# Performance work log

Measured on AMD Instinct MI355X. Metric: run time of the kernel, lower is better.

The kernel has to match this reference:

```python
import jax, jax.numpy as jnp
import numpy as np

N, E, DIN, H, EIN, EH, STEPS = 10000, 100000, 64, 64, 16, 128, 3


def setup_inputs() -> dict:
    key = jax.random.key(0)
    ks = jax.random.split(key, 8)
    n_feat = jax.random.normal(ks[0], (N, DIN), jnp.float32)
    e_feat = jax.random.normal(ks[1], (E, EIN), jnp.float32)
    src = jax.random.randint(ks[2], (E,), 0, N, jnp.int32)
    dst = jax.random.randint(ks[3], (E,), 0, N, jnp.int32)
    W0 = jax.random.normal(ks[4], (DIN, H), jnp.float32) / np.sqrt(DIN)
    b0 = jnp.zeros((H,), jnp.float32)
    We1 = jax.random.normal(ks[5], (EIN, EH), jnp.float32) / np.sqrt(EIN)
    be1 = jnp.zeros((EH,), jnp.float32)
    # small scale so per-edge HxH weight matrices keep activations stable
    We2 = jax.random.normal(ks[6], (EH, H * H), jnp.float32) * 0.02
    be2 = jnp.zeros((H * H,), jnp.float32)
    conv_bias = jnp.zeros((H,), jnp.float32)
    gamma = jnp.ones((H,), jnp.float32)
    beta = jnp.zeros((H,), jnp.float32)
    return {"n_feat": n_feat, "e_feat": e_feat, "src": src, "dst": dst,
            "W0": W0, "b0": b0, "We1": We1, "be1": be1, "We2": We2,
            "be2": be2, "conv_bias": conv_bias, "gamma": gamma, "beta": beta}


def reference(n_feat, e_feat, src, dst, W0, b0, We1, be1, We2, be2, conv_bias, gamma, beta):
    n = n_feat.shape[0]
    h = W0.shape[1]
    out = jax.nn.relu(n_feat @ W0 + b0)  # [N,H]
    # edge network (eval mode: dropout = identity); e_feat is fixed so the
    # per-edge weight matrices are identical each step -> compute once.
    w_edge = (jax.nn.relu(e_feat @ We1 + be1) @ We2 + be2).reshape(-1, h, h)  # [E,H,H]
    for _ in range(STEPS):
        msg = jnp.einsum('ei,eio->eo', out[src], w_edge)  # gather + per-edge matmul
        agg = jax.ops.segment_sum(msg, dst, num_segments=n)  # scatter-sum to dst
        out = jax.nn.relu(agg + conv_bias)
    # BatchNorm1d over nodes (training-mode batch statistics)
    mean = jnp.mean(out, axis=0)
    var = jnp.var(out, axis=0)
    return (out - mean) * jax.lax.rsqrt(var + 1e-5) * gamma + beta
```

## Files before the change

### kernel.cpp

```cpp
#include <hip/hip_runtime.h>
#include <stdint.h>

#define DIN   64
#define HDIM  64
#define EIN   16
#define EHID  128
#define HH    4096
#define TC    8256
#define STEPS 3

typedef short bf16x8 __attribute__((ext_vector_type(8)));
typedef float f32x4  __attribute__((ext_vector_type(4)));

__device__ __forceinline__ unsigned short f32_to_bf16(float f) {
    union { float f; uint32_t u; } v; v.f = f;
    uint32_t r = v.u + 0x7fffu + ((v.u >> 16) & 1u);
    return (unsigned short)(r >> 16);
}
__device__ __forceinline__ float bfu_to_f(unsigned short u) {
    union { uint32_t u; float f; } v; v.u = (uint32_t)u << 16; return v.f;
}

__global__ void k_pro(const float* __restrict__ nf, const float* __restrict__ W0,
                      const float* __restrict__ b0, float* __restrict__ outb,
                      unsigned short* __restrict__ outbf,
                      const float* __restrict__ ef, const float* __restrict__ We1,
                      const float* __restrict__ be1, unsigned short* __restrict__ h,
                      const float* __restrict__ We2, const float* __restrict__ be2,
                      unsigned short* __restrict__ BmatT,
                      const int* __restrict__ src, const int* __restrict__ dst,
                      int* __restrict__ cntS, int* __restrict__ cntD,
                      int n_nodes, int n_edges, int nbN, int nbE, int nbB) {
    __shared__ float smem[DIN * HDIM];
    int b = blockIdx.x, tid = threadIdx.x;
    if (b < nbN) {
        for (int i = tid; i < DIN * HDIM; i += 256) smem[i] = W0[i];
        __syncthreads();
        int node = b * 4 + (tid >> 6);
        int o = tid & 63;
        if (node >= n_nodes) return;
        float xr = nf[node * DIN + o];
        float acc = b0[o];
#pragma unroll 8
        for (int i = 0; i < DIN; ++i)
            acc += __shfl(xr, i, 64) * smem[i * HDIM + o];
        float v = fmaxf(acc, 0.f);
        outb[node * HDIM + o] = v;
        outbf[node * HDIM + o] = f32_to_bf16(v);
    } else if (b < nbN + nbE) {
        int wave = tid >> 6, lane = tid & 63;
        int r = lane & 15, q = lane >> 4;
        int e0 = (b - nbN) * 64 + wave * 16;
        if (e0 >= n_edges) return;
        bf16x8 afr = (bf16x8){};
        bf16x8 bfr[8];
#pragma unroll
        for (int nt = 0; nt < 8; ++nt) bfr[nt] = (bf16x8){};
        if (q < 2) {
            int ea = e0 + r; if (ea >= n_edges) ea = n_edges - 1;
            const float* xa = ef + (size_t)ea * EIN + q * 8;
#pragma unroll
            for (int j = 0; j < 8; ++j) afr[j] = (short)f32_to_bf16(xa[j]);
#pragma unroll
            for (int nt = 0; nt < 8; ++nt)
#pragma unroll
                for (int j = 0; j < 8; ++j)
                    bfr[nt][j] = (short)f32_to_bf16(We1[(q * 8 + j) * EHID + nt * 16 + r]);
        }
        f32x4 acc[8];
#pragma unroll
        for (int nt = 0; nt < 8; ++nt)
            acc[nt] = __builtin_amdgcn_mfma_f32_16x16x32_bf16(afr, bfr[nt], (f32x4){}, 0, 0, 0);
        float bias[8];
#pragma unroll
        for (int nt = 0; nt < 8; ++nt) bias[nt] = be1[nt * 16 + r];
#pragma unroll
        for (int rg = 0; rg < 4; ++rg) {
            int e = e0 + q * 4 + rg;
            if (e >= n_edges) continue;
            ushort4 pk0, pk1;
            pk0.x = f32_to_bf16(fmaxf(acc[0][rg] + bias[0], 0.f));
            pk0.y = f32_to_bf16(fmaxf(acc[1][rg] + bias[1], 0.f));
            pk0.z = f32_to_bf16(fmaxf(acc[2][rg] + bias[2], 0.f));
            pk0.w = f32_to_bf16(fmaxf(acc[3][rg] + bias[3], 0.f));
            pk1.x = f32_to_bf16(fmaxf(acc[4][rg] + bias[4], 0.f));
            pk1.y = f32_to_bf16(fmaxf(acc[5][rg] + bias[5], 0.f));
            pk1.z = f32_to_bf16(fmaxf(acc[6][rg] + bias[6], 0.f));
            pk1.w = f32_to_bf16(fmaxf(acc[7][rg] + bias[7], 0.f));
            *(ushort4*)(h + (size_t)e * EHID + 4 * r) = pk0;
            *(ushort4*)(h + (size_t)e * EHID + 64 + 4 * r) = pk1;
        }
    } else if (b < nbN + nbE + nbB) {
        int t = (b - nbN - nbE) * 256 + tid;
        if (t >= TC * 64) return;
        int c = t >> 6, i = t & 63;
        int m;
        if (c < 8192) {
            int g = c & 127;
            m = (c & ~127) + 8 * (g & 15) + (g >> 4);
        } else {
            int g = c & 63;
            m = (c & ~63) + 4 * (g & 15) + (g >> 4);
        }
        float v;
        if (m < 8192) {
            int p = ((m >> 11) << 5) | (m & 31);
            int k = (p & 64) + ((p & 3) << 4) + ((p >> 2) & 15);
            int o = (m >> 5) & 63;
            v = We2[k * HH + i * 64 + o];
        } else {
            v = be2[i * 64 + (m - 8192)];
        }
        BmatT[t] = f32_to_bf16(v);
    } else {
        int e = (b - nbN - nbE - nbB) * 256 + tid;
        if (e >= n_edges) return;
        atomicAdd(&cntS[src[e]], 1);
        atomicAdd(&cntD[dst[e]], 1);
    }
}

__global__ void k_T(const unsigned short* __restrict__ outbf, const unsigned short* __restrict__ BmatT,
                    unsigned short* __restrict__ T, int n0, int n1) {
    int wave = threadIdx.x >> 6, lane = threadIdx.x & 63;
    int r = lane & 15, q = lane >> 4;
    int eb = n0 + blockIdx.y * 128;
    if (blockIdx.x < 16) {
        int cb = blockIdx.x * 512 + wave * 128;
        bf16x8 bfr[8][2];
#pragma unroll
        for (int nt = 0; nt < 8; ++nt) {
            size_t cofs = (size_t)(cb + nt * 16 + r) * 64;
            bfr[nt][0] = *(const bf16x8*)(BmatT + cofs + q * 8);
            bfr[nt][1] = *(const bf16x8*)(BmatT + cofs + 32 + q * 8);
        }
#pragma unroll
        for (int mt = 0; mt < 8; ++mt) {
            int e = eb + mt * 16 + r;
            if (e >= n1) e = n1 - 1;
            bf16x8 afr0 = *(const bf16x8*)(outbf + (size_t)e * 64 + q * 8);
            bf16x8 afr1 = *(const bf16x8*)(outbf + (size_t)e * 64 + 32 + q * 8);
            f32x4 acc[8];
#pragma unroll
            for (int nt = 0; nt < 8; ++nt) {
                acc[nt] = __builtin_amdgcn_mfma_f32_16x16x32_bf16(afr0, bfr[nt][0], (f32x4){}, 0, 0, 0);
                acc[nt] = __builtin_amdgcn_mfma_f32_16x16x32_bf16(afr1, bfr[nt][1], acc[nt], 0, 0, 0);
            }
#pragma unroll
            for (int rg = 0; rg < 4; ++rg) {
                int n = eb + mt * 16 + q * 4 + rg;
                if (n >= n1) continue;
                ushort4 pa, pb;
                pa.x = f32_to_bf16(acc[0][rg]); pa.y = f32_to_bf16(acc[1][rg]);
                pa.z = f32_to_bf16(acc[2][rg]); pa.w = f32_to_bf16(acc[3][rg]);
                pb.x = f32_to_bf16(acc[4][rg]); pb.y = f32_to_bf16(acc[5][rg]);
                pb.z = f32_to_bf16(acc[6][rg]); pb.w = f32_to_bf16(acc[7][rg]);
                uint4 pk = { ((uint32_t)pa.y << 16) | pa.x, ((uint32_t)pa.w << 16) | pa.z,
                             ((uint32_t)pb.y << 16) | pb.x, ((uint32_t)pb.w << 16) | pb.z };
                *(uint4*)(T + (size_t)(n - n0) * TC + cb + 8 * r) = pk;
            }
        }
    } else {
        if (wave != 0) return;
        int cb = 8192;
        bf16x8 bfr[4][2];
#pragma unroll
        for (int nt = 0; nt < 4; ++nt) {
            size_t cofs = (size_t)(cb + nt * 16 + r) * 64;
            bfr[nt][0] = *(const bf16x8*)(BmatT + cofs + q * 8);
            bfr[nt][1] = *(const bf16x8*)(BmatT + cofs + 32 + q * 8);
        }
#pragma unroll
        for (int mt = 0; mt < 8; ++mt) {
            int e = eb + mt * 16 + r;
            if (e >= n1) e = n1 - 1;
            bf16x8 afr0 = *(const bf16x8*)(outbf + (size_t)e * 64 + q * 8);
            bf16x8 afr1 = *(const bf16x8*)(outbf + (size_t)e * 64 + 32 + q * 8);
            f32x4 acc[4];
#pragma unroll
            for (int nt = 0; nt < 4; ++nt) {
                acc[nt] = __builtin_amdgcn_mfma_f32_16x16x32_bf16(afr0, bfr[nt][0], (f32x4){}, 0, 0, 0);
                acc[nt] = __builtin_amdgcn_mfma_f32_16x16x32_bf16(afr1, bfr[nt][1], acc[nt], 0, 0, 0);
            }
#pragma unroll
            for (int rg = 0; rg < 4; ++rg) {
                int n = eb + mt * 16 + q * 4 + rg;
                if (n >= n1) continue;
                ushort4 pk;
                pk.x = f32_to_bf16(acc[0][rg]);
                pk.y = f32_to_bf16(acc[1][rg]);
                pk.z = f32_to_bf16(acc[2][rg]);
                pk.w = f32_to_bf16(acc[3][rg]);
                *(ushort4*)(T + (size_t)(n - n0) * TC + cb + 4 * r) = pk;
            }
        }
    }
}

__global__ void k_msg(const unsigned short* __restrict__ h, const unsigned short* __restrict__ T,
                      const int* __restrict__ offS, const int* __restrict__ permS,
                      float* __restrict__ msg, int n0, int n1) {
    int wave = threadIdx.x >> 6, lane = threadIdx.x & 63;
    int n = n0 + blockIdx.x * 4 + wave;
    if (n >= n1) return;
    int beg = offS[n], end = offS[n + 1];
    if (beg == end) return;
    int r = lane & 15, q = lane >> 4;
    const unsigned short* Tb = T + (size_t)(n - n0) * TC;
    float bias[4];
#pragma unroll
    for (int nt = 0; nt < 4; ++nt)
        bias[nt] = bfu_to_f(Tb[8192 + nt * 16 + r]);
    for (int j0 = beg; j0 < end; j0 += 16) {
        int jc = j0 + r; if (jc >= end) jc = end - 1;
        int e = permS[jc];
        const unsigned short* he = h + (size_t)e * EHID;
        f32x4 acc[4] = {};
#pragma unroll
        for (int s = 0; s < 4; ++s) {
            bf16x8 afr = *(const bf16x8*)(he + s * 32 + q * 8);
#pragma unroll
            for (int nt = 0; nt < 4; ++nt) {
                bf16x8 bfr = *(const bf16x8*)(Tb + s * 2048 + (nt * 16 + r) * 32 + q * 8);
                acc[nt] = __builtin_amdgcn_mfma_f32_16x16x32_bf16(afr, bfr, acc[nt], 0, 0, 0);
            }
        }
#pragma unroll
        for (int rg = 0; rg < 4; ++rg) {
            int jr = j0 + q * 4 + rg;
            if (jr >= end) continue;
            int er = permS[jr];
            f32x4 pk = { acc[0][rg] + bias[0], acc[1][rg] + bias[1],
                         acc[2][rg] + bias[2], acc[3][rg] + bias[3] };
            *(f32x4*)(msg + (size_t)er * 64 + 4 * r) = pk;
        }
    }
}

__global__ void k_scan(const int* __restrict__ cntS, const int* __restrict__ cntD,
                       int* __restrict__ offS, int* __restrict__ offD,
                       int* __restrict__ curS, int* __restrict__ curD, int n, int total) {
    const int* cnt = blockIdx.x ? cntD : cntS;
    int* off = blockIdx.x ? offD : offS;
    int* cur = blockIdx.x ? curD : curS;
    __shared__ int part[256];
    int tid = threadIdx.x;
    int chunk = (n + 255) / 256;
    int c0 = tid * chunk, c1 = c0 + chunk; if (c1 > n) c1 = n; if (c0 > n) c0 = n;
    int s = 0;
    for (int i = c0; i < c1; ++i) s += cnt[i];
    part[tid] = s;
    __syncthreads();
    for (int st = 1; st < 256; st <<= 1) {
        int v = (tid >= st) ? part[tid - st] : 0;
        __syncthreads();
        part[tid] += v;
        __syncthreads();
    }
    int run = tid ? part[tid - 1] : 0;
    for (int i = c0; i < c1; ++i) { off[i] = run; cur[i] = run; run += cnt[i]; }
    if (tid == 0) off[n] = total;
}

__global__ void k_perm(const int* __restrict__ src, const int* __restrict__ dst,
                       int* __restrict__ curS, int* __restrict__ curD,
                       int* __restrict__ permS, int* __restrict__ permD, int n_edges) {
    int e = blockIdx.x * 256 + threadIdx.x;
    if (e >= n_edges) return;
    permS[atomicAdd(&curS[src[e]], 1)] = e;
    permD[atomicAdd(&curD[dst[e]], 1)] = e;
}

__global__ void k_agg(const float* __restrict__ msg, const int* __restrict__ offD,
                      const int* __restrict__ permD, const float* __restrict__ cbias,
                      float* __restrict__ outb, unsigned short* __restrict__ outbf, int n_nodes) {
    int wave = threadIdx.x >> 6, lane = threadIdx.x & 63;
    int d = blockIdx.x * 4 + wave;
    if (d >= n_nodes) return;
    int o = (lane & 3) * 16 + (lane >> 2);
    float acc = 0.f;
    int end = offD[d + 1];
    for (int j = offD[d]; j < end; ++j)
        acc += msg[(size_t)permD[j] * 64 + lane];
    float v = fmaxf(acc + cbias[o], 0.f);
    outb[(size_t)d * 64 + o] = v;
    outbf[(size_t)d * 64 + o] = f32_to_bf16(v);
}

__global__ void k_bn_stats(const float* __restrict__ out, float* __restrict__ stat, int n_nodes) {
    __shared__ float s1[256], s2[256];
    int tid = threadIdx.x;
    int f = tid & 63, g = tid >> 6;
    float sum = 0.f, ss = 0.f;
    for (int r = blockIdx.x * 4 + g; r < n_nodes; r += 256) {
        float v = out[r * HDIM + f];
        sum += v; ss += v * v;
    }
    s1[tid] = sum; s2[tid] = ss;
    __syncthreads();
    if (tid < 64) {
        float A = s1[tid] + s1[64 + tid] + s1[128 + tid] + s1[192 + tid];
        float B = s2[tid] + s2[64 + tid] + s2[128 + tid] + s2[192 + tid];
        atomicAdd(&stat[tid], A);
        atomicAdd(&stat[64 + tid], B);
    }
}

__global__ void k_bn_apply(const float* __restrict__ out, const float* __restrict__ stat,
                           const float* __restrict__ gamma, const float* __restrict__ beta,
                           float* __restrict__ y, int n, int n_nodes) {
    int t = blockIdx.x * 256 + threadIdx.x;
    if (t >= n) return;
    int f = t & 63;
    float mean = stat[f] / n_nodes;
    float var  = stat[64 + f] / n_nodes - mean * mean;
    float inv  = rsqrtf(var + 1e-5f);
    float scale = gamma[f] * inv;
    float shift = beta[f] - mean * scale;
    y[t] = out[t] * scale + shift;
}

extern "C" void kernel_launch(void* const* d_in, const int* in_sizes, int n_in,
                              void* d_out, int out_size, void* d_ws, size_t ws_size,
                              hipStream_t stream) {
    const float* nf    = (const float*)d_in[0];
    const float* ef    = (const float*)d_in[1];
    const int*   src   = (const int*)d_in[2];
    const int*   dst   = (const int*)d_in[3];
    const float* W0    = (const float*)d_in[4];
    const float* b0    = (const float*)d_in[5];
    const float* We1   = (const float*)d_in[6];
    const float* be1   = (const float*)d_in[7];
    const float* We2   = (const float*)d_in[8];
    const float* be2   = (const float*)d_in[9];
    const float* cbias = (const float*)d_in[10];
    const float* gamma = (const float*)d_in[11];
    const float* beta  = (const float*)d_in[12];
    (void)n_in; (void)out_size;

    int n_nodes = in_sizes[0] / DIN;
    int n_edges = in_sizes[2];

    char* ws = (char*)d_ws;
    size_t off = 0;
    auto carve = [&](size_t bytes) -> void* {
        void* p = ws + off;
        off = (off + bytes + 255) & ~(size_t)255;
        return p;
    };
    unsigned short* h     = (unsigned short*)carve((size_t)n_edges * EHID * 2);
    float*          msg   = (float*)carve((size_t)n_edges * 64 * 4);
    float*          outb  = (float*)carve((size_t)n_nodes * HDIM * 4);
    unsigned short* outbf = (unsigned short*)carve((size_t)n_nodes * HDIM * 2);
    unsigned short* BmatT = (unsigned short*)carve((size_t)TC * 64 * 2);
    int*            offS  = (int*)carve((size_t)(n_nodes + 1) * 4);
    int*            offD  = (int*)carve((size_t)(n_nodes + 1) * 4);
    int*            curS  = (int*)carve((size_t)n_nodes * 4);
    int*            curD  = (int*)carve((size_t)n_nodes * 4);
    int*            permS = (int*)carve((size_t)n_edges * 4);
    int*            permD = (int*)carve((size_t)n_edges * 4);
    float*          stat  = (float*)carve(128 * 4 + (size_t)2 * n_nodes * 4);
    int*            cntS  = (int*)(stat + 128);
    int*            cntD  = cntS + n_nodes;
    unsigned short* T     = (unsigned short*)(ws + off);
    size_t avail = ws_size > off ? ws_size - off : 0;
    long tcap = (long)(avail / ((size_t)TC * 2));
    if (tcap > n_nodes) tcap = n_nodes;
    if (tcap < 64) tcap = 64;
    long tchunk = tcap;

    hipMemsetAsync(stat, 0, 128 * 4 + (size_t)2 * n_nodes * 4, stream);

    int nbN = (n_nodes + 3) / 4;
    int nbE = (n_edges + 63) / 64;
    int nbB = (TC * 64 + 255) / 256;
    int nbH = (n_edges + 255) / 256;
    k_pro<<<dim3(nbN + nbE + nbB + nbH), 256, 0, stream>>>(
        nf, W0, b0, outb, outbf, ef, We1, be1, h, We2, be2, BmatT,
        src, dst, cntS, cntD, n_nodes, n_edges, nbN, nbE, nbB);
    k_scan<<<dim3(2), 256, 0, stream>>>(cntS, cntD, offS, offD, curS, curD, n_nodes, n_edges);
    k_perm<<<dim3((n_edges + 255) / 256), 256, 0, stream>>>(src, dst, curS, curD, permS, permD, n_edges);

    for (int step = 0; step < STEPS; ++step) {
        for (long n0 = 0; n0 < n_nodes; n0 += tchunk) {
            long n1 = n0 + tchunk; if (n1 > n_nodes) n1 = n_nodes;
            long cnt = n1 - n0;
            k_T<<<dim3(17, (cnt + 127) / 128), 256, 0, stream>>>(
                outbf, BmatT, T, (int)n0, (int)n1);
            k_msg<<<dim3((cnt + 3) / 4), 256, 0, stream>>>(
                h, T, offS, permS, msg, (int)n0, (int)n1);
        }
        k_agg<<<dim3((n_nodes + 3) / 4), 256, 0, stream>>>(msg, offD, permD, cbias, outb, outbf, n_nodes);
    }

    k_bn_stats<<<dim3(64), 256, 0, stream>>>(outb, stat, n_nodes);
    k_bn_apply<<<dim3((n_nodes * HDIM + 255) / 256), 256, 0, stream>>>(
        outb, stat, gamma, beta, (float*)d_out, n_nodes * HDIM, n_nodes);
}
```

Measured before the change: 428.7 us.

## Fuse per-node T computation and edge message matmul via LDS staging

Replaces the two-kernel pipeline (k_T writing a large per-node T matrix to global memory, then k_msg reading it back) with a single kernel that computes each 16-node block's T slice in four output chunks into shared memory and immediately consumes it for the outgoing edges. This removes the global round trip of roughly 16 KB per node per step and the chunked launches. BmatT layout and the output column order in msg/k_agg are reorganised to match, and an XOR swizzle is added to the LDS stores. In exchange, each block recomputes through 4 sequential chunks with barriers, edges are spread over waves by round-robin, which may be unbalanced, and the 64 KB+ of LDS per block limits occupancy.

```diff
diff --git a/kernel.cpp b/kernel.cpp
--- a/kernel.cpp
+++ b/kernel.cpp
@@ -93,25 +93,18 @@
     } else if (b < nbN + nbE + nbB) {
         int t = (b - nbN - nbE) * 256 + tid;
         if (t >= TC * 64) return;
-        int c = t >> 6, i = t & 63;
-        int m;
-        if (c < 8192) {
-            int g = c & 127;
-            m = (c & ~127) + 8 * (g & 15) + (g >> 4);
-        } else {
-            int g = c & 63;
-            m = (c & ~63) + 4 * (g & 15) + (g >> 4);
-        }
+        int m = t >> 6, i = t & 63;
         float v;
         if (m < 8192) {
-            int p = ((m >> 11) << 5) | (m & 31);
-            int k = (p & 64) + ((p & 3) << 4) + ((p >> 2) & 15);
-            int o = (m >> 5) & 63;
+            int oc = m >> 11, c2 = m & 2047;
+            int o  = oc * 16 + (c2 >> 7);
+            int K  = ((c2 & 15) << 3) | ((c2 >> 4) & 7);
+            int k  = (K & 64) + ((K & 3) << 4) + ((K >> 2) & 15);
             v = We2[k * HH + i * 64 + o];
         } else {
             v = be2[i * 64 + (m - 8192)];
         }
-        BmatT[t] = f32_to_bf16(v);
+        BmatT[m * 64 + i] = f32_to_bf16(v);
     } else {
         int e = (b - nbN - nbE - nbB) * 256 + tid;
         if (e >= n_edges) return;
@@ -120,119 +113,84 @@
     }
 }
 
-__global__ void k_T(const unsigned short* __restrict__ outbf, const unsigned short* __restrict__ BmatT,
-                    unsigned short* __restrict__ T, int n0, int n1) {
+__global__ void k_fused(const unsigned short* __restrict__ outbf,
+                        const unsigned short* __restrict__ BmatT,
+                        const unsigned short* __restrict__ h,
+                        const int* __restrict__ offS, const int* __restrict__ permS,
+                        float* __restrict__ msg, int n_nodes) {
+    __shared__ short Tlds[16 * 2048];
+    __shared__ float Tb[16 * 64];
     int wave = threadIdx.x >> 6, lane = threadIdx.x & 63;
     int r = lane & 15, q = lane >> 4;
-    int eb = n0 + blockIdx.y * 128;
-    if (blockIdx.x < 16) {
-        int cb = blockIdx.x * 512 + wave * 128;
-        bf16x8 bfr[8][2];
-#pragma unroll
-        for (int nt = 0; nt < 8; ++nt) {
-            size_t cofs = (size_t)(cb + nt * 16 + r) * 64;
-            bfr[nt][0] = *(const bf16x8*)(BmatT + cofs + q * 8);
-            bfr[nt][1] = *(const bf16x8*)(BmatT + cofs + 32 + q * 8);
-        }
-#pragma unroll
-        for (int mt = 0; mt < 8; ++mt) {
-            int e = eb + mt * 16 + r;
-            if (e >= n1) e = n1 - 1;
-            bf16x8 afr0 = *(const bf16x8*)(outbf + (size_t)e * 64 + q * 8);
-            bf16x8 afr1 = *(const bf16x8*)(outbf + (size_t)e * 64 + 32 + q * 8);
-            f32x4 acc[8];
+    int n0 = blockIdx.x * 16;
+
+    int na = n0 + r; if (na >= n_nodes) na = n_nodes - 1;
+    bf16x8 afr0 = *(const bf16x8*)(outbf + (size_t)na * 64 + q * 8);
+    bf16x8 afr1 = *(const bf16x8*)(outbf + (size_t)na * 64 + 32 + q * 8);
+
+    {
+        size_t cofs = (size_t)(8192 + wave * 16 + r) * 64;
+        bf16x8 bb0 = *(const bf16x8*)(BmatT + cofs + q * 8);
+        bf16x8 bb1 = *(const bf16x8*)(BmatT + cofs + 32 + q * 8);
+        f32x4 accB = __builtin_amdgcn_mfma_f32_16x16x32_bf16(afr0, bb0, (f32x4){}, 0, 0, 0);
+        accB = __builtin_amdgcn_mfma_f32_16x16x32_bf16(afr1, bb1, accB, 0, 0, 0);
+#pragma unroll
+        for (int rg = 0; rg < 4; ++rg)
+            Tb[(q * 4 + rg) * 64 + wave * 16 + r] = accB[rg];
+    }
+
+    int nlim = n_nodes - n0; if (nlim > 16) nlim = 16;
+
+    for (int oc = 0; oc < 4; ++oc) {
+        __syncthreads();
+#pragma unroll
+        for (int og = 0; og < 4; ++og) {
+            int o_in = wave * 4 + og;
+            f32x4 a8[8];
 #pragma unroll
             for (int nt = 0; nt < 8; ++nt) {
-                acc[nt] = __builtin_amdgcn_mfma_f32_16x16x32_bf16(afr0, bfr[nt][0], (f32x4){}, 0, 0, 0);
-                acc[nt] = __builtin_amdgcn_mfma_f32_16x16x32_bf16(afr1, bfr[nt][1], acc[nt], 0, 0, 0);
+                size_t cofs = (size_t)(oc * 2048 + (o_in * 8 + nt) * 16 + r) * 64;
+                bf16x8 bv0 = *(const bf16x8*)(BmatT + cofs + q * 8);
+                bf16x8 bv1 = *(const bf16x8*)(BmatT + cofs + 32 + q * 8);
+                a8[nt] = __builtin_amdgcn_mfma_f32_16x16x32_bf16(afr0, bv0, (f32x4){}, 0, 0, 0);
+                a8[nt] = __builtin_amdgcn_mfma_f32_16x16x32_bf16(afr1, bv1, a8[nt], 0, 0, 0);
             }
 #pragma unroll
             for (int rg = 0; rg < 4; ++rg) {
-                int n = eb + mt * 16 + q * 4 + rg;
-                if (n >= n1) continue;
-                ushort4 pa, pb;
-                pa.x = f32_to_bf16(acc[0][rg]); pa.y = f32_to_bf16(acc[1][rg]);
-                pa.z = f32_to_bf16(acc[2][rg]); pa.w = f32_to_bf16(acc[3][rg]);
-                pb.x = f32_to_bf16(acc[4][rg]); pb.y = f32_to_bf16(acc[5][rg]);
-                pb.z = f32_to_bf16(acc[6][rg]); pb.w = f32_to_bf16(acc[7][rg]);
-                uint4 pk = { ((uint32_t)pa.y << 16) | pa.x, ((uint32_t)pa.w << 16) | pa.z,
-                             ((uint32_t)pb.y << 16) | pb.x, ((uint32_t)pb.w << 16) | pb.z };
-                *(uint4*)(T + (size_t)(n - n0) * TC + cb + 8 * r) = pk;
+                bf16x8 pk;
+#pragma unroll
+                for (int nt = 0; nt < 8; ++nt)
+                    pk[nt] = (short)f32_to_bf16(a8[nt][rg]);
+                *(bf16x8*)((char*)Tlds + ((q * 4 + rg) << 12) + (o_in << 8)
+                           + (((r ^ (o_in & 7)) & 15) << 4)) = pk;
             }
         }
-    } else {
-        if (wave != 0) return;
-        int cb = 8192;
-        bf16x8 bfr[4][2];
-#pragma unroll
-        for (int nt = 0; nt < 4; ++nt) {
-            size_t cofs = (size_t)(cb + nt * 16 + r) * 64;
-            bfr[nt][0] = *(const bf16x8*)(BmatT + cofs + q * 8);
-            bfr[nt][1] = *(const bf16x8*)(BmatT + cofs + 32 + q * 8);
-        }
-#pragma unroll
-        for (int mt = 0; mt < 8; ++mt) {
-            int e = eb + mt * 16 + r;
-            if (e >= n1) e = n1 - 1;
-            bf16x8 afr0 = *(const bf16x8*)(outbf + (size_t)e * 64 + q * 8);
-            bf16x8 afr1 = *(const bf16x8*)(outbf + (size_t)e * 64 + 32 + q * 8);
-            f32x4 acc[4];
-#pragma unroll
-            for (int nt = 0; nt < 4; ++nt) {
-                acc[nt] = __builtin_amdgcn_mfma_f32_16x16x32_bf16(afr0, bfr[nt][0], (f32x4){}, 0, 0, 0);
-                acc[nt] = __builtin_amdgcn_mfma_f32_16x16x32_bf16(afr1, bfr[nt][1], acc[nt], 0, 0, 0);
+        __syncthreads();
+        int tt = 0;
+        for (int ni = 0; ni < nlim; ++ni) {
+            int beg = offS[n0 + ni], end = offS[n0 + ni + 1];
+            for (int j0 = beg; j0 < end; j0 += 16, ++tt) {
+                if ((tt & 3) != wave) continue;
+                int jc = j0 + r; if (jc >= end) jc = end - 1;
+                int e = permS[jc];
+                const unsigned short* he = h + (size_t)e * EHID;
+                f32x4 acc = {};
+#pragma unroll
+                for (int ks = 0; ks < 4; ++ks) {
+                    bf16x8 afr = *(const bf16x8*)(he + ks * 32 + q * 8);
+                    bf16x8 bfr = *(const bf16x8*)((char*)Tlds + (ni << 12) + (r << 8)
+                                   + ((((ks * 4 + q) ^ (r & 7)) & 15) << 4));
+                    acc = __builtin_amdgcn_mfma_f32_16x16x32_bf16(afr, bfr, acc, 0, 0, 0);
+                }
+                float bias = Tb[ni * 64 + oc * 16 + r];
+#pragma unroll
+                for (int rg = 0; rg < 4; ++rg) {
+                    int jr = j0 + q * 4 + rg;
+                    if (jr >= end) continue;
+                    int er = permS[jr];
+                    msg[(size_t)er * 64 + oc * 16 + r] = acc[rg] + bias;
+                }
             }
-#pragma unroll
-            for (int rg = 0; rg < 4; ++rg) {
-                int n = eb + mt * 16 + q * 4 + rg;
-                if (n >= n1) continue;
-                ushort4 pk;
-                pk.x = f32_to_bf16(acc[0][rg]);
-                pk.y = f32_to_bf16(acc[1][rg]);
-                pk.z = f32_to_bf16(acc[2][rg]);
-                pk.w = f32_to_bf16(acc[3][rg]);
-                *(ushort4*)(T + (size_t)(n - n0) * TC + cb + 4 * r) = pk;
-            }
-        }
-    }
-}
-
-__global__ void k_msg(const unsigned short* __restrict__ h, const unsigned short* __restrict__ T,
-                      const int* __restrict__ offS, const int* __restrict__ permS,
-                      float* __restrict__ msg, int n0, int n1) {
-    int wave = threadIdx.x >> 6, lane = threadIdx.x & 63;
-    int n = n0 + blockIdx.x * 4 + wave;
-    if (n >= n1) return;
-    int beg = offS[n], end = offS[n + 1];
-    if (beg == end) return;
-    int r = lane & 15, q = lane >> 4;
-    const unsigned short* Tb = T + (size_t)(n - n0) * TC;
-    float bias[4];
-#pragma unroll
-    for (int nt = 0; nt < 4; ++nt)
-        bias[nt] = bfu_to_f(Tb[8192 + nt * 16 + r]);
-    for (int j0 = beg; j0 < end; j0 += 16) {
-        int jc = j0 + r; if (jc >= end) jc = end - 1;
-        int e = permS[jc];
-        const unsigned short* he = h + (size_t)e * EHID;
-        f32x4 acc[4] = {};
-#pragma unroll
-        for (int s = 0; s < 4; ++s) {
-            bf16x8 afr = *(const bf16x8*)(he + s * 32 + q * 8);
-#pragma unroll
-            for (int nt = 0; nt < 4; ++nt) {
-                bf16x8 bfr = *(const bf16x8*)(Tb + s * 2048 + (nt * 16 + r) * 32 + q * 8);
-                acc[nt] = __builtin_amdgcn_mfma_f32_16x16x32_bf16(afr, bfr, acc[nt], 0, 0, 0);
-            }
-        }
-#pragma unroll
-        for (int rg = 0; rg < 4; ++rg) {
-            int jr = j0 + q * 4 + rg;
-            if (jr >= end) continue;
-            int er = permS[jr];
-            f32x4 pk = { acc[0][rg] + bias[0], acc[1][rg] + bias[1],
-                         acc[2][rg] + bias[2], acc[3][rg] + bias[3] };
-            *(f32x4*)(msg + (size_t)er * 64 + 4 * r) = pk;
         }
     }
 }
@@ -277,14 +235,13 @@
     int wave = threadIdx.x >> 6, lane = threadIdx.x & 63;
     int d = blockIdx.x * 4 + wave;
     if (d >= n_nodes) return;
-    int o = (lane & 3) * 16 + (lane >> 2);
     float acc = 0.f;
     int end = offD[d + 1];
     for (int j = offD[d]; j < end; ++j)
         acc += msg[(size_t)permD[j] * 64 + lane];
-    float v = fmaxf(acc + cbias[o], 0.f);
-    outb[(size_t)d * 64 + o] = v;
-    outbf[(size_t)d * 64 + o] = f32_to_bf16(v);
+    float v = fmaxf(acc + cbias[lane], 0.f);
+    outb[(size_t)d * 64 + lane] = v;
+    outbf[(size_t)d * 64 + lane] = f32_to_bf16(v);
 }
 
 __global__ void k_bn_stats(const float* __restrict__ out, float* __restrict__ stat, int n_nodes) {
@@ -336,7 +293,7 @@
     const float* cbias = (const float*)d_in[10];
     const float* gamma = (const float*)d_in[11];
     const float* beta  = (const float*)d_in[12];
-    (void)n_in; (void)out_size;
+    (void)n_in; (void)out_size; (void)ws_size;
 
     int n_nodes = in_sizes[0] / DIN;
     int n_edges = in_sizes[2];
@@ -362,12 +319,6 @@
     float*          stat  = (float*)carve(128 * 4 + (size_t)2 * n_nodes * 4);
     int*            cntS  = (int*)(stat + 128);
     int*            cntD  = cntS + n_nodes;
-    unsigned short* T     = (unsigned short*)(ws + off);
-    size_t avail = ws_size > off ? ws_size - off : 0;
-    long tcap = (long)(avail / ((size_t)TC * 2));
-    if (tcap > n_nodes) tcap = n_nodes;
-    if (tcap < 64) tcap = 64;
-    long tchunk = tcap;
 
     hipMemsetAsync(stat, 0, 128 * 4 + (size_t)2 * n_nodes * 4, stream);
 
@@ -381,15 +332,9 @@
     k_scan<<<dim3(2), 256, 0, stream>>>(cntS, cntD, offS, offD, curS, curD, n_nodes, n_edges);
     k_perm<<<dim3((n_edges + 255) / 256), 256, 0, stream>>>(src, dst, curS, curD, permS, permD, n_edges);
 
+    int nbF = (n_nodes + 15) / 16;
     for (int step = 0; step < STEPS; ++step) {
-        for (long n0 = 0; n0 < n_nodes; n0 += tchunk) {
-            long n1 = n0 + tchunk; if (n1 > n_nodes) n1 = n_nodes;
-            long cnt = n1 - n0;
-            k_T<<<dim3(17, (cnt + 127) / 128), 256, 0, stream>>>(
-                outbf, BmatT, T, (int)n0, (int)n1);
-            k_msg<<<dim3((cnt + 3) / 4), 256, 0, stream>>>(
-                h, T, offS, permS, msg, (int)n0, (int)n1);
-        }
+        k_fused<<<dim3(nbF), 256, 0, stream>>>(outbf, BmatT, h, offS, permS, msg, n_nodes);
         k_agg<<<dim3((n_nodes + 3) / 4), 256, 0, stream>>>(msg, offD, permD, cbias, outb, outbf, n_nodes);
     }
 
```

New measurement: 732.4 us. +70.8%, slower.

## Stage T tile stores through swizzled LDS and store messages in bf16

Applied to the files above, without the earlier changes.

k_T now writes its MFMA outputs into a double-buffered, XOR-swizzled shared-memory tile, then each wave writes whole contiguous row segments of T. This replaces the scattered 16-byte stores to rows spaced TC apart with fully coalesced ones. Separately, per-edge messages are stored as bf16 instead of fp32, halving msg write and gather traffic in k_msg and k_agg. The cost is one block barrier per mt iteration plus extra bf16 rounding error in the messages before they are summed.

```diff
diff --git a/kernel.cpp b/kernel.cpp
--- a/kernel.cpp
+++ b/kernel.cpp
@@ -122,6 +122,7 @@
 
 __global__ void k_T(const unsigned short* __restrict__ outbf, const unsigned short* __restrict__ BmatT,
                     unsigned short* __restrict__ T, int n0, int n1) {
+    __shared__ uint4 stile[2][16 * 64];
     int wave = threadIdx.x >> 6, lane = threadIdx.x & 63;
     int r = lane & 15, q = lane >> 4;
     int eb = n0 + blockIdx.y * 128;
@@ -134,7 +135,6 @@
             bfr[nt][0] = *(const bf16x8*)(BmatT + cofs + q * 8);
             bfr[nt][1] = *(const bf16x8*)(BmatT + cofs + 32 + q * 8);
         }
-#pragma unroll
         for (int mt = 0; mt < 8; ++mt) {
             int e = eb + mt * 16 + r;
             if (e >= n1) e = n1 - 1;
@@ -146,10 +146,10 @@
                 acc[nt] = __builtin_amdgcn_mfma_f32_16x16x32_bf16(afr0, bfr[nt][0], (f32x4){}, 0, 0, 0);
                 acc[nt] = __builtin_amdgcn_mfma_f32_16x16x32_bf16(afr1, bfr[nt][1], acc[nt], 0, 0, 0);
             }
+            uint4* buf = stile[mt & 1];
 #pragma unroll
             for (int rg = 0; rg < 4; ++rg) {
-                int n = eb + mt * 16 + q * 4 + rg;
-                if (n >= n1) continue;
+                int row = q * 4 + rg;
                 ushort4 pa, pb;
                 pa.x = f32_to_bf16(acc[0][rg]); pa.y = f32_to_bf16(acc[1][rg]);
                 pa.z = f32_to_bf16(acc[2][rg]); pa.w = f32_to_bf16(acc[3][rg]);
@@ -157,7 +157,17 @@
                 pb.z = f32_to_bf16(acc[6][rg]); pb.w = f32_to_bf16(acc[7][rg]);
                 uint4 pk = { ((uint32_t)pa.y << 16) | pa.x, ((uint32_t)pa.w << 16) | pa.z,
                              ((uint32_t)pb.y << 16) | pb.x, ((uint32_t)pb.w << 16) | pb.z };
-                *(uint4*)(T + (size_t)(n - n0) * TC + cb + 8 * r) = pk;
+                buf[row * 64 + ((wave * 16 + r) ^ (row & 7))] = pk;
+            }
+            __syncthreads();
+#pragma unroll
+            for (int rr = 0; rr < 4; ++rr) {
+                int row = wave * 4 + rr;
+                int n = eb + mt * 16 + row;
+                if (n < n1) {
+                    uint4 v = buf[row * 64 + (lane ^ (row & 7))];
+                    *(uint4*)(T + (size_t)(n - n0) * TC + blockIdx.x * 512 + lane * 8) = v;
+                }
             }
         }
     } else {
@@ -199,7 +209,7 @@
 
 __global__ void k_msg(const unsigned short* __restrict__ h, const unsigned short* __restrict__ T,
                       const int* __restrict__ offS, const int* __restrict__ permS,
-                      float* __restrict__ msg, int n0, int n1) {
+                      unsigned short* __restrict__ msg, int n0, int n1) {
     int wave = threadIdx.x >> 6, lane = threadIdx.x & 63;
     int n = n0 + blockIdx.x * 4 + wave;
     if (n >= n1) return;
@@ -230,9 +240,12 @@
             int jr = j0 + q * 4 + rg;
             if (jr >= end) continue;
             int er = permS[jr];
-            f32x4 pk = { acc[0][rg] + bias[0], acc[1][rg] + bias[1],
-                         acc[2][rg] + bias[2], acc[3][rg] + bias[3] };
-            *(f32x4*)(msg + (size_t)er * 64 + 4 * r) = pk;
+            ushort4 pk;
+            pk.x = f32_to_bf16(acc[0][rg] + bias[0]);
+            pk.y = f32_to_bf16(acc[1][rg] + bias[1]);
+            pk.z = f32_to_bf16(acc[2][rg] + bias[2]);
+            pk.w = f32_to_bf16(acc[3][rg] + bias[3]);
+            *(ushort4*)(msg + (size_t)er * 64 + 4 * r) = pk;
         }
     }
 }
@@ -271,7 +284,7 @@
     permD[atomicAdd(&curD[dst[e]], 1)] = e;
 }
 
-__global__ void k_agg(const float* __restrict__ msg, const int* __restrict__ offD,
+__global__ void k_agg(const unsigned short* __restrict__ msg, const int* __restrict__ offD,
                       const int* __restrict__ permD, const float* __restrict__ cbias,
                       float* __restrict__ outb, unsigned short* __restrict__ outbf, int n_nodes) {
     int wave = threadIdx.x >> 6, lane = threadIdx.x & 63;
@@ -281,7 +294,7 @@
     float acc = 0.f;
     int end = offD[d + 1];
     for (int j = offD[d]; j < end; ++j)
-        acc += msg[(size_t)permD[j] * 64 + lane];
+        acc += bfu_to_f(msg[(size_t)permD[j] * 64 + lane]);
     float v = fmaxf(acc + cbias[o], 0.f);
     outb[(size_t)d * 64 + o] = v;
     outbf[(size_t)d * 64 + o] = f32_to_bf16(v);
@@ -349,7 +362,7 @@
         return p;
     };
     unsigned short* h     = (unsigned short*)carve((size_t)n_edges * EHID * 2);
-    float*          msg   = (float*)carve((size_t)n_edges * 64 * 4);
+    unsigned short* msg   = (unsigned short*)carve((size_t)n_edges * 64 * 2);
     float*          outb  = (float*)carve((size_t)n_nodes * HDIM * 4);
     unsigned short* outbf = (unsigned short*)carve((size_t)n_nodes * HDIM * 2);
     unsigned short* BmatT = (unsigned short*)carve((size_t)TC * 64 * 2);
```

Result: slower. 502.5 us (+17.2%).
